# Performance work log

Hardware: AMD Instinct MI355X
Metric: run time of the kernel (lower is better)

Reference implementation:

```python
import jax, jax.numpy as jnp
import numpy as np


def setup_inputs() -> dict:
    key = jax.random.key(0)
    ks = jax.random.split(key, 12)
    B, N, NF, H = 8, 256, 128, 128
    w = lambda k, shape: jax.random.normal(k, shape, dtype=jnp.float32) * 0.05
    return {
        "node_feat": jax.random.normal(ks[0], (B, N, NF), dtype=jnp.float32),
        "pos": jax.random.normal(ks[1], (B, N, 3), dtype=jnp.float32),
        "valid": jnp.ones((B, N), dtype=jnp.float32),
        "adj": jax.random.uniform(ks[2], (B, N, N), dtype=jnp.float32),
        "ew1": w(ks[3], (2 * NF + 2, H)),
        "ew2": w(ks[4], (H, H)),
        "cw1": w(ks[5], (H, H)),
        "cw2": w(ks[6], (H, 1)),
        "nw1": w(ks[7], (NF + H, H)),
        "nw2": w(ks[8], (H, NF)),
        "iw": w(ks[9], (H, 1)),
    }


def reference(node_feat, pos, valid, adj, ew1, ew2, cw1, cw2, nw1, nw2, iw):
    B, N, NF = node_feat.shape
    # pairwise broadcast features [B,N,N,NF]
    hi = jnp.broadcast_to(node_feat[:, :, None, :], (B, N, N, NF))
    hj = jnp.broadcast_to(node_feat[:, None, :, :], (B, N, N, NF))
    vec = pos[:, :, None, :] - pos[:, None, :, :]          # [B,N,N,3]
    dist = jnp.sum(vec * vec, axis=-1, keepdims=True)       # [B,N,N,1]
    edge_input = jnp.concatenate([hi, hj, dist, adj[..., None]], axis=-1)
    # phi_e: two bias-free linears with SiLU
    m_ij = jax.nn.silu(jax.nn.silu(edge_input @ ew1) @ ew2)  # [B,N,N,H]
    # normalize relative vectors
    norm = jnp.linalg.norm(vec, axis=-1, keepdims=True)
    vec_n = vec / jnp.maximum(norm, 1e-10)
    vmask = valid[:, :, None, None]                          # [B,N,1,1] -> broadcast over j
    # coordinate update (update_pos=True)
    coord = jax.nn.silu(m_ij @ cw1) @ cw2                    # [B,N,N,1]
    pos_new = pos + jnp.mean(vec_n * coord * vmask, axis=2)
    # inference gating (infer=True)
    e_ij = jax.nn.sigmoid(m_ij @ iw)
    m_ij = m_ij * e_ij
    message = jnp.mean(m_ij * vmask, axis=2)                 # [B,N,H]
    node_input = jnp.concatenate([node_feat, message], axis=-1)
    node_new = node_feat + jax.nn.silu(node_input @ nw1) @ nw2
    return pos_new, node_new
```

## Files before the change

kernel.cpp:

```cpp
#include <hip/hip_runtime.h>
#include <hip/hip_bf16.h>


#define BB 8
#define NN 256
#define HD 128
#define JT 64
#define NT (NN/JT)

typedef short bf16x8 __attribute__((ext_vector_type(8)));
typedef float f32x4  __attribute__((ext_vector_type(4)));

__device__ __forceinline__ float sigmoidf_(float x){
    return __builtin_amdgcn_rcpf(1.0f + __expf(-x));
}
__device__ __forceinline__ float siluf_(float x){
    return x * __builtin_amdgcn_rcpf(1.0f + __expf(-x));
}
__device__ __forceinline__ unsigned int cvtpk_bf16(float lo, float hi){
    unsigned int r;
    asm("v_cvt_pk_bf16_f32 %0, %1, %2" : "=v"(r) : "v"(lo), "v"(hi));
    return r;
}
__device__ __forceinline__ unsigned short f2bf(float x){
    unsigned int u = __float_as_uint(x);
    u += 0x7FFF + ((u>>16)&1);
    return (unsigned short)(u>>16);
}
__device__ __forceinline__ float bf2f(unsigned short h){
    return __uint_as_float(((unsigned int)h)<<16);
}

#define MFMA_BF16(d,a,b) d = __builtin_amdgcn_mfma_f32_16x16x32_bf16(a, b, d, 0, 0, 0)


__global__ __launch_bounds__(128) void precompute_T(
    const float* __restrict__ nf, const float* __restrict__ ew1,
    unsigned short* __restrict__ T0, unsigned short* __restrict__ T1)
{
    __shared__ float nfs[HD];
    const int bi = blockIdx.x;
    const int h  = threadIdx.x;
    nfs[h] = nf[(size_t)bi*HD + h];
    __syncthreads();
    float a0 = 0.f, a1 = 0.f;
    #pragma unroll 4
    for (int f = 0; f < HD; ++f){
        const float v = nfs[f];
        a0 = fmaf(v, ew1[f*HD + h],      a0);
        a1 = fmaf(v, ew1[(HD+f)*HD + h], a1);
    }
    T0[bi*HD + h] = f2bf(a0);
    T1[bi*HD + h] = f2bf(a1);
}

__global__ __launch_bounds__(256) void prep_w(
    const float* __restrict__ ew2, const float* __restrict__ cw1,
    unsigned short* __restrict__ dst)
{
    const int e = blockIdx.x*256 + threadIdx.x;
    const int m = e >> 14;
    const int rem = e & 16383;
    const int h = rem >> 7, k = rem & 127;
    if (m == 0)
        dst[rem] = f2bf(ew2[k*HD + h]);
    else
        dst[16384 + ((((h<<7) | k) ^ ((h&7)<<3)))] = f2bf(cw1[k*HD + h]);
}


__global__ __launch_bounds__(256) void egcl_main(
    const float* __restrict__ nf,  const float* __restrict__ pos,
    const float* __restrict__ valid, const float* __restrict__ adj,
    const float* __restrict__ ew1,
    const float* __restrict__ cw2,
    const float* __restrict__ nw1, const float* __restrict__ nw2,
    const float* __restrict__ iw,
    const unsigned short* __restrict__ T0u, const unsigned short* __restrict__ T1u,
    const unsigned short* __restrict__ wE,  const unsigned short* __restrict__ wC,
    float* __restrict__ out)
{
    __shared__ unsigned short sW [16384];
    __shared__ unsigned short sHM[JT*HD];
    __shared__ float gpart[4][JT];
    __shared__ float cpart[4][JT];
    __shared__ float2 d2a[JT];
    __shared__ float msgp[HD];
    __shared__ float red3[3];

    const int tid = threadIdx.x;
    const int bi  = blockIdx.x;
    const int b   = bi >> 8;
    const int wm  = tid >> 6;
    const int l   = tid & 63, lr = l & 15, lg = l >> 4;
    const int hp  = tid & 63,  jq = tid >> 6;
    const int hh  = tid & 127, half = tid >> 7;

    {
        const uint4* g = (const uint4*)wC;
        uint4* s = (uint4*)sW;
        #pragma unroll
        for (int r = 0; r < 8; ++r) s[r*256 + tid] = g[r*256 + tid];
    }

    bf16x8 aE[2][4];
    {
        const unsigned short* pE = wE + (((wm*32 + lr) << 7) + lg*8);
        #pragma unroll
        for (int mt = 0; mt < 2; ++mt)
            #pragma unroll
            for (int kk = 0; kk < 4; ++kk)
                aE[mt][kk] = *(const bf16x8*)(pE + (mt*16 << 7) + kk*32);
    }

    const float t0a = bf2f(T0u[bi*HD + 2*hp]);
    const float t0b = bf2f(T0u[bi*HD + 2*hp + 1]);
    const float w6a = ew1[256*HD + 2*hp], w6b = ew1[256*HD + 2*hp + 1];
    const float w7a = ew1[257*HD + 2*hp], w7b = ew1[257*HD + 2*hp + 1];
    const float pix = pos[bi*3+0], piy = pos[bi*3+1], piz = pos[bi*3+2];
    const float validi = valid[bi];
    const unsigned short* __restrict__ T1b = T1u + (size_t)(b*NN)*HD;
    const float* __restrict__ posb   = pos + (size_t)(b*NN)*3;
    const float* __restrict__ adjrow = adj + (size_t)bi*NN;

    float msgacc[8];
    #pragma unroll
    for (int s = 0; s < 8; ++s) msgacc[s] = 0.f;
    float pax = 0.f, pay = 0.f, paz = 0.f;

    #define D2A_PHASE(tt)                                          \
        if (tid < JT){                                             \
            const int j_ = (tt)*JT + tid;                          \
            const float dx_ = pix - posb[j_*3+0];                  \
            const float dy_ = piy - posb[j_*3+1];                  \
            const float dz_ = piz - posb[j_*3+2];                  \
            d2a[tid] = make_float2(dx_*dx_ + dy_*dy_ + dz_*dz_,    \
                                   adjrow[j_]);                    \
        }

    D2A_PHASE(0)
    __syncthreads();

    for (int t = 0; t < NT; ++t){
        const int j0 = t*JT;

        #pragma unroll 2
        for (int r = 0; r < 16; ++r){
            const int jl = jq*16 + r;
            const int j  = j0 + jl;
            const float2 da = d2a[jl];
            const ushort2 t1v = *(const ushort2*)&T1b[(size_t)j*HD + 2*hp];
            const float s0 = siluf_(fmaf(da.y, w7a, fmaf(da.x, w6a, t0a + bf2f(t1v.x))));
            const float s1 = siluf_(fmaf(da.y, w7b, fmaf(da.x, w6b, t0b + bf2f(t1v.y))));
            ((unsigned int*)sHM)[(jl*64 + hp) ^ ((jl&7)<<2)] = cvtpk_bf16(s0, s1);
        }
        __syncthreads();

        f32x4 acc[2][4];
        #pragma unroll
        for (int mt = 0; mt < 2; ++mt)
            #pragma unroll
            for (int nt = 0; nt < 4; ++nt)
                acc[mt][nt] = (f32x4){0.f,0.f,0.f,0.f};
        {
            __builtin_amdgcn_s_setprio(1);
            #pragma unroll
            for (int kk = 0; kk < 4; ++kk){
                const int kb = kk*32 + lg*8;
                bf16x8 bf[4];
                #pragma unroll
                for (int nt = 0; nt < 4; ++nt){
                    const int jb = nt*16 + lr;
                    bf[nt] = *(const bf16x8*)&sHM[((jb<<7) + kb) ^ ((jb&7)<<3)];
                }
                #pragma unroll
                for (int mt = 0; mt < 2; ++mt)
                    #pragma unroll
                    for (int nt = 0; nt < 4; ++nt)
                        MFMA_BF16(acc[mt][nt], aE[mt][kk], bf[nt]);
            }
            __builtin_amdgcn_s_setprio(0);
        }
        __syncthreads();

        {
            float pg[4] = {0.f,0.f,0.f,0.f};
            #pragma unroll
            for (int mt = 0; mt < 2; ++mt){
                const f32x4 iwv = *(const f32x4*)&iw[wm*32 + mt*16 + lg*4];
                #pragma unroll
                for (int nt = 0; nt < 4; ++nt){
                    #pragma unroll
                    for (int i = 0; i < 4; ++i){
                        acc[mt][nt][i] = siluf_(acc[mt][nt][i]);
                        pg[nt] = fmaf(acc[mt][nt][i], iwv[i], pg[nt]);
                    }
                    const int jr = nt*16 + lr;
                    uint2 mv;
                    mv.x = cvtpk_bf16(acc[mt][nt][0], acc[mt][nt][1]);
                    mv.y = cvtpk_bf16(acc[mt][nt][2], acc[mt][nt][3]);
                    *(uint2*)&sHM[((jr<<7) + wm*32 + mt*16 + lg*4) ^ ((jr&7)<<3)] = mv;
                }
            }
            #pragma unroll
            for (int nt = 0; nt < 4; ++nt){
                pg[nt] += __shfl_xor(pg[nt], 16);
                pg[nt] += __shfl_xor(pg[nt], 32);
            }
            if (lg == 0){
                #pragma unroll
                for (int nt = 0; nt < 4; ++nt)
                    gpart[wm][nt*16 + lr] = pg[nt];
            }
        }
        __syncthreads();

        #pragma unroll
        for (int nt = 0; nt < 4; ++nt){
            const int jr = nt*16 + lr;
            const float g = sigmoidf_(gpart[0][jr]+gpart[1][jr]+gpart[2][jr]+gpart[3][jr]);
            #pragma unroll
            for (int mt = 0; mt < 2; ++mt)
                #pragma unroll
                for (int i = 0; i < 4; ++i)
                    msgacc[mt*4+i] = fmaf(acc[mt][nt][i], g, msgacc[mt*4+i]);
        }

        #pragma unroll
        for (int mt = 0; mt < 2; ++mt)
            #pragma unroll
            for (int nt = 0; nt < 4; ++nt)
                acc[mt][nt] = (f32x4){0.f,0.f,0.f,0.f};
        {
            __builtin_amdgcn_s_setprio(1);
            #pragma unroll
            for (int kk = 0; kk < 4; ++kk){
                const int kb = kk*32 + lg*8;
                bf16x8 af[2];
                #pragma unroll
                for (int mt = 0; mt < 2; ++mt){
                    const int hr = wm*32 + mt*16 + lr;
                    af[mt] = *(const bf16x8*)&sW[((hr<<7) + kb) ^ ((hr&7)<<3)];
                }
                bf16x8 bf[4];
                #pragma unroll
                for (int nt = 0; nt < 4; ++nt){
                    const int jb = nt*16 + lr;
                    bf[nt] = *(const bf16x8*)&sHM[((jb<<7) + kb) ^ ((jb&7)<<3)];
                }
                #pragma unroll
                for (int mt = 0; mt < 2; ++mt)
                    #pragma unroll
                    for (int nt = 0; nt < 4; ++nt)
                        MFMA_BF16(acc[mt][nt], af[mt], bf[nt]);
            }
            __builtin_amdgcn_s_setprio(0);
        }
        {
            float pc[4] = {0.f,0.f,0.f,0.f};
            #pragma unroll
            for (int mt = 0; mt < 2; ++mt){
                const f32x4 cwv = *(const f32x4*)&cw2[wm*32 + mt*16 + lg*4];
                #pragma unroll
                for (int nt = 0; nt < 4; ++nt)
                    #pragma unroll
                    for (int i = 0; i < 4; ++i)
                        pc[nt] = fmaf(siluf_(acc[mt][nt][i]), cwv[i], pc[nt]);
            }
            #pragma unroll
            for (int nt = 0; nt < 4; ++nt){
                pc[nt] += __shfl_xor(pc[nt], 16);
                pc[nt] += __shfl_xor(pc[nt], 32);
            }
            if (lg == 0){
                #pragma unroll
                for (int nt = 0; nt < 4; ++nt)
                    cpart[wm][nt*16 + lr] = pc[nt];
            }
        }

        if (t < NT-1) D2A_PHASE(t+1)
        __syncthreads();

        if (tid < JT){
            const float c = cpart[0][tid] + cpart[1][tid] + cpart[2][tid] + cpart[3][tid];
            const int j = j0 + tid;
            const float pjx = posb[j*3+0], pjy = posb[j*3+1], pjz = posb[j*3+2];
            const float dx = pix-pjx, dy = piy-pjy, dz = piz-pjz;
            const float d2 = dx*dx + dy*dy + dz*dz;
            const float nrm = __builtin_amdgcn_sqrtf(d2);
            const float inv = __builtin_amdgcn_rcpf(fmaxf(nrm, 1e-10f));
            const float cd = c * inv;
            pax = fmaf(dx, cd, pax);
            pay = fmaf(dy, cd, pay);
            paz = fmaf(dz, cd, paz);
        }
    }

    #pragma unroll
    for (int s = 0; s < 8; ++s){
        msgacc[s] += __shfl_xor(msgacc[s], 1);
        msgacc[s] += __shfl_xor(msgacc[s], 2);
        msgacc[s] += __shfl_xor(msgacc[s], 4);
        msgacc[s] += __shfl_xor(msgacc[s], 8);
    }
    if (lr == 0){
        #pragma unroll
        for (int mt = 0; mt < 2; ++mt)
            #pragma unroll
            for (int i = 0; i < 4; ++i)
                msgp[wm*32 + mt*16 + lg*4 + i] = msgacc[mt*4+i];
    }

    if (wm == 0){
        float sx = pax, sy = pay, sz = paz;
        #pragma unroll
        for (int off = 1; off <= 32; off <<= 1){
            sx += __shfl_xor(sx, off);
            sy += __shfl_xor(sy, off);
            sz += __shfl_xor(sz, off);
        }
        if (l == 0){ red3[0] = sx; red3[1] = sy; red3[2] = sz; }
    }
    __syncthreads();

    float* nbuf = (float*)sW;
    float* ni   = nbuf;
    float* n1l  = nbuf + 256;
    float* np2  = nbuf + 384;

    const float scale = validi * (1.0f/NN);
    if (tid < HD){
        ni[tid]      = nf[(size_t)bi*HD + tid];
        ni[HD + tid] = msgp[tid] * scale;
    }
    if (tid == 0){
        out[(size_t)bi*3+0] = pix + red3[0]*scale;
        out[(size_t)bi*3+1] = piy + red3[1]*scale;
        out[(size_t)bi*3+2] = piz + red3[2]*scale;
    }
    __syncthreads();

    float p1 = 0.f;
    for (int f = 0; f < HD; ++f){
        const int ff = half*HD + f;
        p1 = fmaf(ni[ff], nw1[ff*HD + hh], p1);
    }
    np2[half*HD + hh] = p1;
    __syncthreads();
    if (tid < HD) n1l[tid] = siluf_(np2[tid] + np2[HD + tid]);
    __syncthreads();
    float p2 = 0.f;
    for (int k = 0; k < 64; ++k){
        const int kk2 = half*64 + k;
        p2 = fmaf(n1l[kk2], nw2[kk2*HD + hh], p2);
    }
    np2[half*HD + hh] = p2;
    __syncthreads();
    if (tid < HD){
        out[(size_t)BB*NN*3 + (size_t)bi*HD + tid] =
            nf[(size_t)bi*HD + tid] + np2[tid] + np2[HD + tid];
    }
}

extern "C" void kernel_launch(void* const* d_in, const int* in_sizes, int n_in,
                              void* d_out, int out_size, void* d_ws, size_t ws_size,
                              hipStream_t stream)
{
    const float* nf    = (const float*)d_in[0];
    const float* pos   = (const float*)d_in[1];
    const float* valid = (const float*)d_in[2];
    const float* adj   = (const float*)d_in[3];
    const float* ew1   = (const float*)d_in[4];
    const float* ew2   = (const float*)d_in[5];
    const float* cw1   = (const float*)d_in[6];
    const float* cw2   = (const float*)d_in[7];
    const float* nw1   = (const float*)d_in[8];
    const float* nw2   = (const float*)d_in[9];
    const float* iw    = (const float*)d_in[10];
    float* out = (float*)d_out;

    unsigned short* wE  = (unsigned short*)d_ws;
    unsigned short* wC  = wE + 16384;
    unsigned short* T0u = wC + 16384;
    unsigned short* T1u = T0u + (size_t)BB*NN*HD;

    hipLaunchKernelGGL(prep_w, dim3(128), dim3(256), 0, stream, ew2, cw1, wE);
    hipLaunchKernelGGL(precompute_T, dim3(BB*NN), dim3(HD), 0, stream,
                       nf, ew1, T0u, T1u);
    hipLaunchKernelGGL(egcl_main, dim3(BB*NN), dim3(256), 0, stream,
                       nf, pos, valid, adj, ew1, cw2, nw1, nw2, iw,
                       T0u, T1u, wE, wC, out);
}
```

Measured before the change: 154.9 us.

## Software-pipeline phase-1 edge hidden computation across j-tiles with split LDS buffers

```diff
diff --git a/kernel.cpp b/kernel.cpp
--- a/kernel.cpp
+++ b/kernel.cpp
@@ -81,10 +81,11 @@
     float* __restrict__ out)
 {
     __shared__ unsigned short sW [16384];
-    __shared__ unsigned short sHM[JT*HD];
+    __shared__ unsigned short sH1[JT*HD];
+    __shared__ unsigned short sM [JT*HD];
     __shared__ float gpart[4][JT];
     __shared__ float cpart[4][JT];
-    __shared__ float2 d2a[JT];
+    __shared__ float2 d2a[2][JT];
     __shared__ float msgp[HD];
     __shared__ float red3[3];
 
@@ -128,40 +129,52 @@
     for (int s = 0; s < 8; ++s) msgacc[s] = 0.f;
     float pax = 0.f, pay = 0.f, paz = 0.f;
 
-    #define D2A_PHASE(tt)                                          \
+    #define D2A_PHASE(tt, buf)                                     \
         if (tid < JT){                                             \
             const int j_ = (tt)*JT + tid;                          \
             const float dx_ = pix - posb[j_*3+0];                  \
             const float dy_ = piy - posb[j_*3+1];                  \
             const float dz_ = piz - posb[j_*3+2];                  \
-            d2a[tid] = make_float2(dx_*dx_ + dy_*dy_ + dz_*dz_,    \
-                                   adjrow[j_]);                    \
-        }
-
-    D2A_PHASE(0)
-    __syncthreads();
+            d2a[buf][tid] = make_float2(dx_*dx_ + dy_*dy_ + dz_*dz_, \
+                                        adjrow[j_]);               \
+        }
+
+    #define P1_COMPUTE(tt, buf, ph)                                             \
+        _Pragma("unroll")                                                       \
+        for (int r = 0; r < 16; ++r){                                           \
+            const int jl = jq*16 + r;                                           \
+            const float2 da = d2a[buf][jl];                                     \
+            const ushort2 t1v = *(const ushort2*)&T1b[(size_t)((tt)*JT + jl)*HD + 2*hp]; \
+            const float s0 = siluf_(fmaf(da.y, w7a, fmaf(da.x, w6a, t0a + bf2f(t1v.x)))); \
+            const float s1 = siluf_(fmaf(da.y, w7b, fmaf(da.x, w6b, t0b + bf2f(t1v.y)))); \
+            ph[r] = cvtpk_bf16(s0, s1);                                         \
+        }
+
+    #define P1_WRITE(ph)                                                        \
+        _Pragma("unroll")                                                       \
+        for (int r = 0; r < 16; ++r){                                           \
+            const int jl = jq*16 + r;                                           \
+            ((unsigned int*)sH1)[(jl*64 + hp) ^ ((jl&7)<<2)] = ph[r];           \
+        }
+
+    unsigned int ph[16];
+
+    D2A_PHASE(0, 0)
+    __syncthreads();
+    P1_COMPUTE(0, 0, ph)
+    P1_WRITE(ph)
 
     for (int t = 0; t < NT; ++t){
-        const int j0 = t*JT;
-
-        #pragma unroll 2
-        for (int r = 0; r < 16; ++r){
-            const int jl = jq*16 + r;
-            const int j  = j0 + jl;
-            const float2 da = d2a[jl];
-            const ushort2 t1v = *(const ushort2*)&T1b[(size_t)j*HD + 2*hp];
-            const float s0 = siluf_(fmaf(da.y, w7a, fmaf(da.x, w6a, t0a + bf2f(t1v.x))));
-            const float s1 = siluf_(fmaf(da.y, w7b, fmaf(da.x, w6b, t0b + bf2f(t1v.y))));
-            ((unsigned int*)sHM)[(jl*64 + hp) ^ ((jl&7)<<2)] = cvtpk_bf16(s0, s1);
-        }
         __syncthreads();
 
-        f32x4 acc[2][4];
+        if (t < NT-1) D2A_PHASE(t+1, (t+1)&1)
+
+        f32x4 acc1[2][4];
         #pragma unroll
         for (int mt = 0; mt < 2; ++mt)
             #pragma unroll
             for (int nt = 0; nt < 4; ++nt)
-                acc[mt][nt] = (f32x4){0.f,0.f,0.f,0.f};
+                acc1[mt][nt] = (f32x4){0.f,0.f,0.f,0.f};
         {
             __builtin_amdgcn_s_setprio(1);
             #pragma unroll
@@ -171,17 +184,16 @@
                 #pragma unroll
                 for (int nt = 0; nt < 4; ++nt){
                     const int jb = nt*16 + lr;
-                    bf[nt] = *(const bf16x8*)&sHM[((jb<<7) + kb) ^ ((jb&7)<<3)];
+                    bf[nt] = *(const bf16x8*)&sH1[((jb<<7) + kb) ^ ((jb&7)<<3)];
                 }
                 #pragma unroll
                 for (int mt = 0; mt < 2; ++mt)
                     #pragma unroll
                     for (int nt = 0; nt < 4; ++nt)
-                        MFMA_BF16(acc[mt][nt], aE[mt][kk], bf[nt]);
+                        MFMA_BF16(acc1[mt][nt], aE[mt][kk], bf[nt]);
             }
             __builtin_amdgcn_s_setprio(0);
         }
-        __syncthreads();
 
         {
             float pg[4] = {0.f,0.f,0.f,0.f};
@@ -192,14 +204,14 @@
                 for (int nt = 0; nt < 4; ++nt){
                     #pragma unroll
                     for (int i = 0; i < 4; ++i){
-                        acc[mt][nt][i] = siluf_(acc[mt][nt][i]);
-                        pg[nt] = fmaf(acc[mt][nt][i], iwv[i], pg[nt]);
+                        acc1[mt][nt][i] = siluf_(acc1[mt][nt][i]);
+                        pg[nt] = fmaf(acc1[mt][nt][i], iwv[i], pg[nt]);
                     }
                     const int jr = nt*16 + lr;
                     uint2 mv;
-                    mv.x = cvtpk_bf16(acc[mt][nt][0], acc[mt][nt][1]);
-                    mv.y = cvtpk_bf16(acc[mt][nt][2], acc[mt][nt][3]);
-                    *(uint2*)&sHM[((jr<<7) + wm*32 + mt*16 + lg*4) ^ ((jr&7)<<3)] = mv;
+                    mv.x = cvtpk_bf16(acc1[mt][nt][0], acc1[mt][nt][1]);
+                    mv.y = cvtpk_bf16(acc1[mt][nt][2], acc1[mt][nt][3]);
+                    *(uint2*)&sM[((jr<<7) + wm*32 + mt*16 + lg*4) ^ ((jr&7)<<3)] = mv;
                 }
             }
             #pragma unroll
@@ -215,22 +227,12 @@
         }
         __syncthreads();
 
-        #pragma unroll
-        for (int nt = 0; nt < 4; ++nt){
-            const int jr = nt*16 + lr;
-            const float g = sigmoidf_(gpart[0][jr]+gpart[1][jr]+gpart[2][jr]+gpart[3][jr]);
-            #pragma unroll
-            for (int mt = 0; mt < 2; ++mt)
-                #pragma unroll
-                for (int i = 0; i < 4; ++i)
-                    msgacc[mt*4+i] = fmaf(acc[mt][nt][i], g, msgacc[mt*4+i]);
-        }
-
+        f32x4 acc2[2][4];
         #pragma unroll
         for (int mt = 0; mt < 2; ++mt)
             #pragma unroll
             for (int nt = 0; nt < 4; ++nt)
-                acc[mt][nt] = (f32x4){0.f,0.f,0.f,0.f};
+                acc2[mt][nt] = (f32x4){0.f,0.f,0.f,0.f};
         {
             __builtin_amdgcn_s_setprio(1);
             #pragma unroll
@@ -246,16 +248,30 @@
                 #pragma unroll
                 for (int nt = 0; nt < 4; ++nt){
                     const int jb = nt*16 + lr;
-                    bf[nt] = *(const bf16x8*)&sHM[((jb<<7) + kb) ^ ((jb&7)<<3)];
+                    bf[nt] = *(const bf16x8*)&sM[((jb<<7) + kb) ^ ((jb&7)<<3)];
                 }
                 #pragma unroll
                 for (int mt = 0; mt < 2; ++mt)
                     #pragma unroll
                     for (int nt = 0; nt < 4; ++nt)
-                        MFMA_BF16(acc[mt][nt], af[mt], bf[nt]);
+                        MFMA_BF16(acc2[mt][nt], af[mt], bf[nt]);
             }
             __builtin_amdgcn_s_setprio(0);
         }
+
+        #pragma unroll
+        for (int nt = 0; nt < 4; ++nt){
+            const int jr = nt*16 + lr;
+            const float g = sigmoidf_(gpart[0][jr]+gpart[1][jr]+gpart[2][jr]+gpart[3][jr]);
+            #pragma unroll
+            for (int mt = 0; mt < 2; ++mt)
+                #pragma unroll
+                for (int i = 0; i < 4; ++i)
+                    msgacc[mt*4+i] = fmaf(acc1[mt][nt][i], g, msgacc[mt*4+i]);
+        }
+
+        if (t < NT-1) P1_COMPUTE(t+1, (t+1)&1, ph)
+
         {
             float pc[4] = {0.f,0.f,0.f,0.f};
             #pragma unroll
@@ -265,7 +281,7 @@
                 for (int nt = 0; nt < 4; ++nt)
                     #pragma unroll
                     for (int i = 0; i < 4; ++i)
-                        pc[nt] = fmaf(siluf_(acc[mt][nt][i]), cwv[i], pc[nt]);
+                        pc[nt] = fmaf(siluf_(acc2[mt][nt][i]), cwv[i], pc[nt]);
             }
             #pragma unroll
             for (int nt = 0; nt < 4; ++nt){
@@ -278,13 +294,13 @@
                     cpart[wm][nt*16 + lr] = pc[nt];
             }
         }
-
-        if (t < NT-1) D2A_PHASE(t+1)
         __syncthreads();
+
+        if (t < NT-1) P1_WRITE(ph)
 
         if (tid < JT){
             const float c = cpart[0][tid] + cpart[1][tid] + cpart[2][tid] + cpart[3][tid];
-            const int j = j0 + tid;
+            const int j = t*JT + tid;
             const float pjx = posb[j*3+0], pjy = posb[j*3+1], pjz = posb[j*3+2];
             const float dx = pix-pjx, dy = piy-pjy, dz = piz-pjz;
             const float d2 = dx*dx + dy*dy + dz*dz;
```

Result: slower. 199.0 us (+28.4%).

## Split hidden/message LDS buffers and double-buffer d2a to drop a barrier

Applied to the files above, without the earlier changes.

```diff
diff --git a/kernel.cpp b/kernel.cpp
--- a/kernel.cpp
+++ b/kernel.cpp
@@ -81,12 +81,13 @@
     float* __restrict__ out)
 {
     __shared__ unsigned short sW [16384];
-    __shared__ unsigned short sHM[JT*HD];
+    __shared__ unsigned short sH1[JT*HD];
+    __shared__ unsigned short sM [JT*HD];
     __shared__ float gpart[4][JT];
     __shared__ float cpart[4][JT];
-    __shared__ float2 d2a[JT];
+    __shared__ float2 d2a[2][JT];
     __shared__ float msgp[HD];
-    __shared__ float red3[3];
+    __shared__ float red3p[4][3];
 
     const int tid = threadIdx.x;
     const int bi  = blockIdx.x;
@@ -128,17 +129,18 @@
     for (int s = 0; s < 8; ++s) msgacc[s] = 0.f;
     float pax = 0.f, pay = 0.f, paz = 0.f;
 
-    #define D2A_PHASE(tt)                                          \
-        if (tid < JT){                                             \
-            const int j_ = (tt)*JT + tid;                          \
+    #define D2A_PHASE(tt, buf)                                     \
+        if (l < 16){                                               \
+            const int jl_ = wm*16 + l;                             \
+            const int j_  = (tt)*JT + jl_;                         \
             const float dx_ = pix - posb[j_*3+0];                  \
             const float dy_ = piy - posb[j_*3+1];                  \
             const float dz_ = piz - posb[j_*3+2];                  \
-            d2a[tid] = make_float2(dx_*dx_ + dy_*dy_ + dz_*dz_,    \
-                                   adjrow[j_]);                    \
-        }
-
-    D2A_PHASE(0)
+            d2a[buf][jl_] = make_float2(dx_*dx_ + dy_*dy_ + dz_*dz_, \
+                                        adjrow[j_]);               \
+        }
+
+    D2A_PHASE(0, 0)
     __syncthreads();
 
     for (int t = 0; t < NT; ++t){
@@ -148,11 +150,11 @@
         for (int r = 0; r < 16; ++r){
             const int jl = jq*16 + r;
             const int j  = j0 + jl;
-            const float2 da = d2a[jl];
+            const float2 da = d2a[t&1][jl];
             const ushort2 t1v = *(const ushort2*)&T1b[(size_t)j*HD + 2*hp];
             const float s0 = siluf_(fmaf(da.y, w7a, fmaf(da.x, w6a, t0a + bf2f(t1v.x))));
             const float s1 = siluf_(fmaf(da.y, w7b, fmaf(da.x, w6b, t0b + bf2f(t1v.y))));
-            ((unsigned int*)sHM)[(jl*64 + hp) ^ ((jl&7)<<2)] = cvtpk_bf16(s0, s1);
+            ((unsigned int*)sH1)[(jl*64 + hp) ^ ((jl&7)<<2)] = cvtpk_bf16(s0, s1);
         }
         __syncthreads();
 
@@ -171,7 +173,7 @@
                 #pragma unroll
                 for (int nt = 0; nt < 4; ++nt){
                     const int jb = nt*16 + lr;
-                    bf[nt] = *(const bf16x8*)&sHM[((jb<<7) + kb) ^ ((jb&7)<<3)];
+                    bf[nt] = *(const bf16x8*)&sH1[((jb<<7) + kb) ^ ((jb&7)<<3)];
                 }
                 #pragma unroll
                 for (int mt = 0; mt < 2; ++mt)
@@ -181,7 +183,6 @@
             }
             __builtin_amdgcn_s_setprio(0);
         }
-        __syncthreads();
 
         {
             float pg[4] = {0.f,0.f,0.f,0.f};
@@ -199,7 +200,7 @@
                     uint2 mv;
                     mv.x = cvtpk_bf16(acc[mt][nt][0], acc[mt][nt][1]);
                     mv.y = cvtpk_bf16(acc[mt][nt][2], acc[mt][nt][3]);
-                    *(uint2*)&sHM[((jr<<7) + wm*32 + mt*16 + lg*4) ^ ((jr&7)<<3)] = mv;
+                    *(uint2*)&sM[((jr<<7) + wm*32 + mt*16 + lg*4) ^ ((jr&7)<<3)] = mv;
                 }
             }
             #pragma unroll
@@ -246,7 +247,7 @@
                 #pragma unroll
                 for (int nt = 0; nt < 4; ++nt){
                     const int jb = nt*16 + lr;
-                    bf[nt] = *(const bf16x8*)&sHM[((jb<<7) + kb) ^ ((jb&7)<<3)];
+                    bf[nt] = *(const bf16x8*)&sM[((jb<<7) + kb) ^ ((jb&7)<<3)];
                 }
                 #pragma unroll
                 for (int mt = 0; mt < 2; ++mt)
@@ -279,12 +280,13 @@
             }
         }
 
-        if (t < NT-1) D2A_PHASE(t+1)
+        if (t < NT-1) D2A_PHASE(t+1, (t+1)&1)
         __syncthreads();
 
-        if (tid < JT){
-            const float c = cpart[0][tid] + cpart[1][tid] + cpart[2][tid] + cpart[3][tid];
-            const int j = j0 + tid;
+        if (l < 16){
+            const int jl = wm*16 + l;
+            const float c = cpart[0][jl] + cpart[1][jl] + cpart[2][jl] + cpart[3][jl];
+            const int j = j0 + jl;
             const float pjx = posb[j*3+0], pjy = posb[j*3+1], pjz = posb[j*3+2];
             const float dx = pix-pjx, dy = piy-pjy, dz = piz-pjz;
             const float d2 = dx*dx + dy*dy + dz*dz;
@@ -312,15 +314,15 @@
                 msgp[wm*32 + mt*16 + lg*4 + i] = msgacc[mt*4+i];
     }
 
-    if (wm == 0){
+    if (l < 16){
         float sx = pax, sy = pay, sz = paz;
         #pragma unroll
-        for (int off = 1; off <= 32; off <<= 1){
+        for (int off = 1; off <= 8; off <<= 1){
             sx += __shfl_xor(sx, off);
             sy += __shfl_xor(sy, off);
             sz += __shfl_xor(sz, off);
         }
-        if (l == 0){ red3[0] = sx; red3[1] = sy; red3[2] = sz; }
+        if (l == 0){ red3p[wm][0] = sx; red3p[wm][1] = sy; red3p[wm][2] = sz; }
     }
     __syncthreads();
 
@@ -335,9 +337,9 @@
         ni[HD + tid] = msgp[tid] * scale;
     }
     if (tid == 0){
-        out[(size_t)bi*3+0] = pix + red3[0]*scale;
-        out[(size_t)bi*3+1] = piy + red3[1]*scale;
-        out[(size_t)bi*3+2] = piz + red3[2]*scale;
+        out[(size_t)bi*3+0] = pix + (red3p[0][0]+red3p[1][0]+red3p[2][0]+red3p[3][0])*scale;
+        out[(size_t)bi*3+1] = piy + (red3p[0][1]+red3p[1][1]+red3p[2][1]+red3p[3][1])*scale;
+        out[(size_t)bi*3+2] = piz + (red3p[0][2]+red3p[1][2]+red3p[2][2]+red3p[3][2])*scale;
     }
     __syncthreads();
 
```

Measured after the change: 159.1 us. 1.03x slower.
